# Kernel tuning notes

Hardware: AMD Instinct MI355X
Metric: run time of the kernel (lower is better)

The kernel has to match this reference:

```python
import jax, jax.numpy as jnp
import numpy as np

EMBED_DIM = 1024
ATTN_DIM = 128
B, S = 4, 2048


def setup_inputs() -> dict:
    key = jax.random.key(0)
    k1, k2, k3, k4 = jax.random.split(key, 4)
    embedded = jax.random.normal(k1, (B, S, EMBED_DIM), dtype=jnp.float32)
    # torch nn.Linear weights are [out_features, in_features]
    scale = 1.0 / np.sqrt(EMBED_DIM)
    Wk = jax.random.uniform(k2, (ATTN_DIM, EMBED_DIM), dtype=jnp.float32, minval=-scale, maxval=scale)
    Wq = jax.random.uniform(k3, (ATTN_DIM, EMBED_DIM), dtype=jnp.float32, minval=-scale, maxval=scale)
    Wv = jax.random.uniform(k4, (ATTN_DIM, EMBED_DIM), dtype=jnp.float32, minval=-scale, maxval=scale)
    return {"embedded": embedded, "Wk": Wk, "Wq": Wq, "Wv": Wv}


def reference(embedded, Wk, Wq, Wv):
    # projections (no bias): x @ W.T
    k = jnp.einsum('bse,ae->bsa', embedded, Wk)  # [B,S,A]
    q = jnp.einsum('bse,ae->bsa', embedded, Wq)
    v = jnp.einsum('bse,ae->bsa', embedded, Wv)
    ad = k.shape[-1]
    scores = jnp.einsum('bqa,bka->bqk', q, k) / jnp.sqrt(jnp.float32(ad))  # [B,S,S]
    causal = jnp.tril(jnp.ones((scores.shape[1], scores.shape[1]), dtype=bool))
    scores = jnp.where(causal, scores, -jnp.inf)
    probs = jax.nn.softmax(scores, axis=-1)
    out = jnp.einsum('bqk,bka->bqa', probs, v)
    return jnp.round(out, 4)
```

## Files before the change

### kernel.cpp

```cpp
#include <hip/hip_runtime.h>
#include <hip/hip_bf16.h>
#include <math.h>

#define B 4
#define S 2048
#define E 1024
#define A 128
#define CHUNK 256
#define NCHMAX 8

typedef __attribute__((ext_vector_type(8))) short short8;
typedef __attribute__((ext_vector_type(4))) float floatx4;

static __device__ __forceinline__ short f2bf(float f) {
  union { float f; unsigned u; } c;
  c.f = f;
  unsigned r = (c.u + 0x7fffu + ((c.u >> 16) & 1u)) >> 16;
  return (short)r;
}
static __device__ __forceinline__ unsigned f2bf2(float x, float y) {
  __hip_bfloat162 h = __float22bfloat162_rn(float2{x, y});
  union { __hip_bfloat162 h; unsigned u; } c;
  c.h = h;
  return c.u;
}

#define PJ 72
__global__ __launch_bounds__(256) void proj_gemm(
    const float* __restrict__ X,
    const float* __restrict__ Wq,
    const float* __restrict__ Wk,
    const float* __restrict__ Wv,
    short* __restrict__ Qbf,
    short* __restrict__ Kbf,
    short* __restrict__ Vt) {
  __shared__ short As[64 * PJ];
  __shared__ short Bs[128 * PJ];

  const int m0 = blockIdx.x * 64;
  const int which = blockIdx.y;
  const float* Wp = (which == 0) ? Wq : (which == 1) ? Wk : Wv;

  const int tid = threadIdx.x;
  const int wave = tid >> 6;
  const int lane = tid & 63;
  const int mh = wave & 1;
  const int nh = wave >> 1;
  const int l16 = lane & 15;
  const int quad = lane >> 4;

  floatx4 acc[2][4] = {};

  for (int k0 = 0; k0 < E; k0 += 64) {
#pragma unroll
    for (int i = 0; i < 4; ++i) {
      const int f = tid + i * 256;
      const int row = f >> 4, c4 = f & 15;
      const float4 v = *(const float4*)&X[(size_t)(m0 + row) * E + k0 + c4 * 4];
      uint2 p; p.x = f2bf2(v.x, v.y); p.y = f2bf2(v.z, v.w);
      *(uint2*)&As[row * PJ + c4 * 4] = p;
    }
#pragma unroll
    for (int i = 0; i < 8; ++i) {
      const int f = tid + i * 256;
      const int row = f >> 4, c4 = f & 15;
      const float4 v = *(const float4*)&Wp[(size_t)row * E + k0 + c4 * 4];
      uint2 p; p.x = f2bf2(v.x, v.y); p.y = f2bf2(v.z, v.w);
      *(uint2*)&Bs[row * PJ + c4 * 4] = p;
    }
    __syncthreads();

    short8 afr[2][2], bfr[4][2];
#pragma unroll
    for (int ms = 0; ms < 2; ++ms)
#pragma unroll
      for (int ks = 0; ks < 2; ++ks)
        afr[ms][ks] = *(const short8*)&As[(mh * 32 + ms * 16 + l16) * PJ + ks * 32 + quad * 8];
#pragma unroll
    for (int nt = 0; nt < 4; ++nt)
#pragma unroll
      for (int ks = 0; ks < 2; ++ks)
        bfr[nt][ks] = *(const short8*)&Bs[(nh * 64 + nt * 16 + l16) * PJ + ks * 32 + quad * 8];

#pragma unroll
    for (int ms = 0; ms < 2; ++ms)
#pragma unroll
      for (int nt = 0; nt < 4; ++nt)
#pragma unroll
        for (int ks = 0; ks < 2; ++ks)
          acc[ms][nt] = __builtin_amdgcn_mfma_f32_16x16x32_bf16(
              afr[ms][ks], bfr[nt][ks], acc[ms][nt], 0, 0, 0);
    __syncthreads();
  }

  const float qscale = 0.08838834764831845f;
#pragma unroll
  for (int ms = 0; ms < 2; ++ms) {
#pragma unroll
    for (int nt = 0; nt < 4; ++nt) {
      const int n = nh * 64 + nt * 16 + l16;
      const int mbase = m0 + mh * 32 + ms * 16 + quad * 4;
      if (which == 2) {
        const int b = mbase >> 11, s = mbase & (S - 1);
        short4 p;
        p.x = f2bf(acc[ms][nt][0]); p.y = f2bf(acc[ms][nt][1]);
        p.z = f2bf(acc[ms][nt][2]); p.w = f2bf(acc[ms][nt][3]);
        *(short4*)&Vt[((size_t)b * A + n) * S + s] = p;
      } else {
        short* Outp = (which == 0) ? Qbf : Kbf;
        const float sc = (which == 0) ? qscale : 1.0f;
#pragma unroll
        for (int r = 0; r < 4; ++r)
          Outp[(size_t)(mbase + r) * A + n] = f2bf(acc[ms][nt][r] * sc);
      }
    }
  }
}

#define LK 132
#define LV 68
__global__ __launch_bounds__(256) void attn_part(
    const short* __restrict__ Qbf,
    const short* __restrict__ Kbf,
    const short* __restrict__ Vt,
    float* __restrict__ Opart,
    float* __restrict__ Lpart) {
  __shared__ short Ks[64 * LK];
  __shared__ short Vs[128 * LV];
  __shared__ short Ps[4][16 * LV];

  const int rev = (int)gridDim.x - 1 - (int)blockIdx.x;
  const int qt = rev >> 3;
  const int chunk = rev & 7;
  const int b = qt >> 5;
  const int q0 = (qt & 31) << 6;
  const int nk = q0 + 64;
  const int kstart = chunk * CHUNK;
  if (kstart >= nk) return;
  const int kend = min(kstart + CHUNK, nk);

  const int tid = threadIdx.x;
  const int wave = tid >> 6;
  const int lane = tid & 63;
  const int l16 = lane & 15;
  const int quad = lane >> 4;

  short8 qfr[4];
  {
    const size_t qrow = (size_t)(b * S + q0 + wave * 16 + l16);
#pragma unroll
    for (int ks = 0; ks < 4; ++ks)
      qfr[ks] = *(const short8*)&Qbf[qrow * A + ks * 32 + quad * 8];
  }

  float l_acc[4] = {0.f, 0.f, 0.f, 0.f};
  floatx4 oacc[8] = {};

  const int myrow = q0 + wave * 16 + quad * 4;
  const short* Kbase = Kbf + (size_t)b * S * A;
  const short* Vbase = Vt + (size_t)b * A * S;

  for (int j0 = kstart; j0 < kend; j0 += 64) {
#pragma unroll
    for (int i = 0; i < 4; ++i) {
      const int f = tid + i * 256;
      const int row = f >> 4, c8 = f & 15;
      *(short8*)&Ks[row * LK + c8 * 8] =
          *(const short8*)&Kbase[(size_t)(j0 + row) * A + c8 * 8];
    }
#pragma unroll
    for (int i = 0; i < 4; ++i) {
      const int f = tid + i * 256;
      const int ar = f >> 3, c8 = f & 7;
      *(short8*)&Vs[ar * LV + c8 * 8] =
          *(const short8*)&Vbase[(size_t)ar * S + j0 + c8 * 8];
    }
    __syncthreads();

    floatx4 sc[4];
#pragma unroll
    for (int nt = 0; nt < 4; ++nt) {
      floatx4 c = {};
#pragma unroll
      for (int ks = 0; ks < 4; ++ks) {
        const short8 bfr = *(const short8*)&Ks[(nt * 16 + l16) * LK + ks * 32 + quad * 8];
        c = __builtin_amdgcn_mfma_f32_16x16x32_bf16(qfr[ks], bfr, c, 0, 0, 0);
      }
      sc[nt] = c;
    }

#pragma unroll
    for (int nt = 0; nt < 4; ++nt) {
      const int key = j0 + nt * 16 + l16;
#pragma unroll
      for (int r = 0; r < 4; ++r) {
        const float p = (key > myrow + r) ? 0.f : __expf(sc[nt][r]);
        sc[nt][r] = p;
        l_acc[r] += p;
      }
    }

#pragma unroll
    for (int nt = 0; nt < 4; ++nt)
#pragma unroll
      for (int r = 0; r < 4; ++r)
        Ps[wave][(quad * 4 + r) * LV + nt * 16 + l16] = f2bf(sc[nt][r]);

    short8 pfr[2];
#pragma unroll
    for (int ks = 0; ks < 2; ++ks)
      pfr[ks] = *(const short8*)&Ps[wave][l16 * LV + ks * 32 + quad * 8];

#pragma unroll
    for (int nt = 0; nt < 8; ++nt) {
#pragma unroll
      for (int ks = 0; ks < 2; ++ks) {
        const short8 vfr = *(const short8*)&Vs[(nt * 16 + l16) * LV + ks * 32 + quad * 8];
        oacc[nt] = __builtin_amdgcn_mfma_f32_16x16x32_bf16(pfr[ks], vfr, oacc[nt], 0, 0, 0);
      }
    }
    __syncthreads();
  }

  const int slot = qt * NCHMAX + chunk;
  float* op = Opart + (size_t)slot * 64 * 128;
  const int lr = wave * 16 + quad * 4;
#pragma unroll
  for (int nt = 0; nt < 8; ++nt)
#pragma unroll
    for (int r = 0; r < 4; ++r)
      op[(lr + r) * 128 + nt * 16 + l16] = oacc[nt][r];

#pragma unroll
  for (int r = 0; r < 4; ++r) {
    float l = l_acc[r];
    l += __shfl_xor(l, 1);
    l += __shfl_xor(l, 2);
    l += __shfl_xor(l, 4);
    l += __shfl_xor(l, 8);
    if (l16 == 0) Lpart[slot * 64 + lr + r] = l;
  }
}

__global__ __launch_bounds__(256) void attn_reduce(
    const float* __restrict__ Opart,
    const float* __restrict__ Lpart,
    float* __restrict__ Out) {
  const int qt = blockIdx.x;
  const int b = qt >> 5;
  const int q0 = (qt & 31) << 6;
  const int nch = (q0 + 64 + CHUNK - 1) / CHUNK;

  const int tid = threadIdx.x;
  const int lr = tid >> 2;
  const int c0 = (tid & 3) * 32;

  float ltot = 0.f;
  for (int c = 0; c < nch; ++c) ltot += Lpart[(qt * NCHMAX + c) * 64 + lr];
  const float inv = 1.f / ltot;

  float4 acc[8] = {};
  for (int c = 0; c < nch; ++c) {
    const float4* op = (const float4*)
        (Opart + ((size_t)(qt * NCHMAX + c) * 64 + lr) * 128 + c0);
#pragma unroll
    for (int i = 0; i < 8; ++i) {
      const float4 v = op[i];
      acc[i].x += v.x; acc[i].y += v.y; acc[i].z += v.z; acc[i].w += v.w;
    }
  }

  float4* o = (float4*)(Out + (size_t)(b * S + q0 + lr) * A + c0);
#pragma unroll
  for (int i = 0; i < 8; ++i) {
    float4 v = acc[i];
    v.x *= inv; v.y *= inv; v.z *= inv; v.w *= inv;
    o[i] = v;
  }
}

extern "C" void kernel_launch(void* const* d_in, const int* in_sizes, int n_in,
                              void* d_out, int out_size, void* d_ws, size_t ws_size,
                              hipStream_t stream) {
  const float* X  = (const float*)d_in[0];
  const float* Wk = (const float*)d_in[1];
  const float* Wq = (const float*)d_in[2];
  const float* Wv = (const float*)d_in[3];
  float* Out = (float*)d_out;

  const size_t qkv_elems = (size_t)B * S * A;
  short* Qbf = (short*)d_ws;
  short* Kbf = Qbf + qkv_elems;
  short* Vt  = Kbf + qkv_elems;
  float* Opart = (float*)(Vt + qkv_elems);
  float* Lpart = Opart + (size_t)1024 * 64 * 128;

  dim3 pgrid(B * S / 64, 3);
  proj_gemm<<<pgrid, 256, 0, stream>>>(X, Wq, Wk, Wv, Qbf, Kbf, Vt);
  attn_part<<<(B * S / 64) * NCHMAX, 256, 0, stream>>>(Qbf, Kbf, Vt, Opart, Lpart);
  attn_reduce<<<B * S / 64, 256, 0, stream>>>(Opart, Lpart, Out);
}
```

Measured before the change: 136.4 us.

## Compute transposed scores to keep P in registers; pre-convert weights to bf16

The attention kernel now computes S^T (K as the A operand, Q as B), so each lane holds four consecutive keys for one query. It packs exp values straight into bf16 fragments and feeds them to 16x16x16 MFMAs against V, which removes the per-wave LDS round trip for P and the extra barrier-free shuffle of probabilities. A separate small kernel converts the weights to bf16 once per call, so the projection GEMM loads half the bytes and skips per-block conversion. The costs are an extra kernel launch and smaller-K MFMAs (16x16x16) with more instructions for the PV product.

After: 143.8 us. +5.5%, slower.

```diff
diff --git a/kernel.cpp b/kernel.cpp
--- a/kernel.cpp
+++ b/kernel.cpp
@@ -9,8 +9,24 @@
 #define CHUNK 256
 #define NCHMAX 8
 
+typedef __attribute__((ext_vector_type(4))) short shortx4;
 typedef __attribute__((ext_vector_type(8))) short short8;
 typedef __attribute__((ext_vector_type(4))) float floatx4;
+
+#if defined(__has_builtin)
+#if __has_builtin(__builtin_amdgcn_mfma_f32_16x16x16bf16_1k)
+#define MFMA16(Av, Bv, Cv) __builtin_amdgcn_mfma_f32_16x16x16bf16_1k((Av), (Bv), (Cv), 0, 0, 0)
+#endif
+#endif
+#ifndef MFMA16
+static __device__ __forceinline__ floatx4 mfma16_asm(shortx4 a, shortx4 b, floatx4 c) {
+  floatx4 d;
+  asm volatile("v_mfma_f32_16x16x16_bf16 %0, %1, %2, %3"
+               : "=v"(d) : "v"(a), "v"(b), "v"(c));
+  return d;
+}
+#define MFMA16(Av, Bv, Cv) mfma16_asm((Av), (Bv), (Cv))
+#endif
 
 static __device__ __forceinline__ short f2bf(float f) {
   union { float f; unsigned u; } c;
@@ -25,12 +41,24 @@
   return c.u;
 }
 
+__global__ __launch_bounds__(256) void wconv(
+    const float* __restrict__ Wq,
+    const float* __restrict__ Wk,
+    const float* __restrict__ Wv,
+    short* __restrict__ Wbf) {
+  const int which = blockIdx.y;
+  const float* Wp = (which == 0) ? Wq : (which == 1) ? Wk : Wv;
+  short* o = Wbf + (size_t)which * A * E;
+  const int f = blockIdx.x * 256 + threadIdx.x;
+  const float4 v = *(const float4*)&Wp[(size_t)f * 4];
+  uint2 p; p.x = f2bf2(v.x, v.y); p.y = f2bf2(v.z, v.w);
+  *(uint2*)&o[(size_t)f * 4] = p;
+}
+
 #define PJ 72
 __global__ __launch_bounds__(256) void proj_gemm(
     const float* __restrict__ X,
-    const float* __restrict__ Wq,
-    const float* __restrict__ Wk,
-    const float* __restrict__ Wv,
+    const short* __restrict__ Wbf,
     short* __restrict__ Qbf,
     short* __restrict__ Kbf,
     short* __restrict__ Vt) {
@@ -39,7 +67,7 @@
 
   const int m0 = blockIdx.x * 64;
   const int which = blockIdx.y;
-  const float* Wp = (which == 0) ? Wq : (which == 1) ? Wk : Wv;
+  const short* Wpb = Wbf + (size_t)which * A * E;
 
   const int tid = threadIdx.x;
   const int wave = tid >> 6;
@@ -61,12 +89,11 @@
       *(uint2*)&As[row * PJ + c4 * 4] = p;
     }
 #pragma unroll
-    for (int i = 0; i < 8; ++i) {
+    for (int i = 0; i < 4; ++i) {
       const int f = tid + i * 256;
-      const int row = f >> 4, c4 = f & 15;
-      const float4 v = *(const float4*)&Wp[(size_t)row * E + k0 + c4 * 4];
-      uint2 p; p.x = f2bf2(v.x, v.y); p.y = f2bf2(v.z, v.w);
-      *(uint2*)&Bs[row * PJ + c4 * 4] = p;
+      const int row = f >> 3, c8 = f & 7;
+      *(short8*)&Bs[row * PJ + c8 * 8] =
+          *(const short8*)&Wpb[(size_t)row * E + k0 + c8 * 8];
     }
     __syncthreads();
 
@@ -127,7 +154,6 @@
     float* __restrict__ Lpart) {
   __shared__ short Ks[64 * LK];
   __shared__ short Vs[128 * LV];
-  __shared__ short Ps[4][16 * LV];
 
   const int rev = (int)gridDim.x - 1 - (int)blockIdx.x;
   const int qt = rev >> 3;
@@ -145,18 +171,19 @@
   const int l16 = lane & 15;
   const int quad = lane >> 4;
 
+  const int qrow = q0 + wave * 16 + l16;
+
   short8 qfr[4];
   {
-    const size_t qrow = (size_t)(b * S + q0 + wave * 16 + l16);
+    const size_t qr = (size_t)(b * S + qrow);
 #pragma unroll
     for (int ks = 0; ks < 4; ++ks)
-      qfr[ks] = *(const short8*)&Qbf[qrow * A + ks * 32 + quad * 8];
-  }
-
-  float l_acc[4] = {0.f, 0.f, 0.f, 0.f};
-  floatx4 oacc[8] = {};
-
-  const int myrow = q0 + wave * 16 + quad * 4;
+      qfr[ks] = *(const short8*)&Qbf[qr * A + ks * 32 + quad * 8];
+  }
+
+  float l_acc = 0.f;
+  floatx4 oaccT[8] = {};
+
   const short* Kbase = Kbf + (size_t)b * S * A;
   const short* Vbase = Vt + (size_t)b * A * S;
 
@@ -177,69 +204,50 @@
     }
     __syncthreads();
 
-    floatx4 sc[4];
 #pragma unroll
     for (int nt = 0; nt < 4; ++nt) {
-      floatx4 c = {};
+      floatx4 st = {};
 #pragma unroll
       for (int ks = 0; ks < 4; ++ks) {
-        const short8 bfr = *(const short8*)&Ks[(nt * 16 + l16) * LK + ks * 32 + quad * 8];
-        c = __builtin_amdgcn_mfma_f32_16x16x32_bf16(qfr[ks], bfr, c, 0, 0, 0);
+        const short8 kfr = *(const short8*)&Ks[(nt * 16 + l16) * LK + ks * 32 + quad * 8];
+        st = __builtin_amdgcn_mfma_f32_16x16x32_bf16(kfr, qfr[ks], st, 0, 0, 0);
       }
-      sc[nt] = c;
-    }
-
-#pragma unroll
-    for (int nt = 0; nt < 4; ++nt) {
-      const int key = j0 + nt * 16 + l16;
+      float pr[4];
 #pragma unroll
       for (int r = 0; r < 4; ++r) {
-        const float p = (key > myrow + r) ? 0.f : __expf(sc[nt][r]);
-        sc[nt][r] = p;
-        l_acc[r] += p;
+        const int key = j0 + nt * 16 + quad * 4 + r;
+        const float p = (key > qrow) ? 0.f : __expf(st[r]);
+        pr[r] = p;
+        l_acc += p;
       }
-    }
-
-#pragma unroll
-    for (int nt = 0; nt < 4; ++nt)
-#pragma unroll
-      for (int r = 0; r < 4; ++r)
-        Ps[wave][(quad * 4 + r) * LV + nt * 16 + l16] = f2bf(sc[nt][r]);
-
-    short8 pfr[2];
-#pragma unroll
-    for (int ks = 0; ks < 2; ++ks)
-      pfr[ks] = *(const short8*)&Ps[wave][l16 * LV + ks * 32 + quad * 8];
-
-#pragma unroll
-    for (int nt = 0; nt < 8; ++nt) {
-#pragma unroll
-      for (int ks = 0; ks < 2; ++ks) {
-        const short8 vfr = *(const short8*)&Vs[(nt * 16 + l16) * LV + ks * 32 + quad * 8];
-        oacc[nt] = __builtin_amdgcn_mfma_f32_16x16x32_bf16(pfr[ks], vfr, oacc[nt], 0, 0, 0);
+      union { uint2 u; shortx4 s; } pk;
+      pk.u.x = f2bf2(pr[0], pr[1]);
+      pk.u.y = f2bf2(pr[2], pr[3]);
+      const shortx4 pfrB = pk.s;
+
+#pragma unroll
+      for (int at = 0; at < 8; ++at) {
+        const shortx4 vfr = *(const shortx4*)&Vs[(at * 16 + l16) * LV + nt * 16 + quad * 4];
+        oaccT[at] = MFMA16(vfr, pfrB, oaccT[at]);
       }
     }
     __syncthreads();
   }
+
+  l_acc += __shfl_xor(l_acc, 16);
+  l_acc += __shfl_xor(l_acc, 32);
 
   const int slot = qt * NCHMAX + chunk;
   float* op = Opart + (size_t)slot * 64 * 128;
-  const int lr = wave * 16 + quad * 4;
-#pragma unroll
-  for (int nt = 0; nt < 8; ++nt)
-#pragma unroll
-    for (int r = 0; r < 4; ++r)
-      op[(lr + r) * 128 + nt * 16 + l16] = oacc[nt][r];
-
-#pragma unroll
-  for (int r = 0; r < 4; ++r) {
-    float l = l_acc[r];
-    l += __shfl_xor(l, 1);
-    l += __shfl_xor(l, 2);
-    l += __shfl_xor(l, 4);
-    l += __shfl_xor(l, 8);
-    if (l16 == 0) Lpart[slot * 64 + lr + r] = l;
-  }
+  const int lr = wave * 16 + l16;
+#pragma unroll
+  for (int at = 0; at < 8; ++at) {
+    float4 v;
+    v.x = oaccT[at][0]; v.y = oaccT[at][1];
+    v.z = oaccT[at][2]; v.w = oaccT[at][3];
+    *(float4*)&op[(size_t)lr * 128 + at * 16 + quad * 4] = v;
+  }
+  if (quad == 0) Lpart[slot * 64 + lr] = l_acc;
 }
 
 __global__ __launch_bounds__(256) void attn_reduce(
@@ -294,9 +302,11 @@
   short* Vt  = Kbf + qkv_elems;
   float* Opart = (float*)(Vt + qkv_elems);
   float* Lpart = Opart + (size_t)1024 * 64 * 128;
-
+  short* Wbf = (short*)(Lpart + (size_t)1024 * 64);
+
+  wconv<<<dim3(A * E / 4 / 256, 3), 256, 0, stream>>>(Wq, Wk, Wv, Wbf);
   dim3 pgrid(B * S / 64, 3);
-  proj_gemm<<<pgrid, 256, 0, stream>>>(X, Wq, Wk, Wv, Qbf, Kbf, Vt);
+  proj_gemm<<<pgrid, 256, 0, stream>>>(X, Wbf, Qbf, Kbf, Vt);
   attn_part<<<(B * S / 64) * NCHMAX, 256, 0, stream>>>(Qbf, Kbf, Vt, Opart, Lpart);
   attn_reduce<<<B * S / 64, 256, 0, stream>>>(Opart, Lpart, Out);
 }
```

## Pre-convert weights to bf16 and register-prefetch next tiles in GEMM and attention

Applied to the files above, without the earlier changes.

Adds a small kernel that converts the three projection weight matrices to bf16 once per call, so the projection GEMM loads half as many weight bytes and skips per-tile conversion. Both the projection GEMM and the attention partial kernel now prefetch the next K-step tile into registers while MFMAs run on the current shared-memory tile, with the barrier moved to the top of the loop. This trades extra register pressure and one more kernel launch for more overlap of global loads with compute.

After: 131.5 us. 1.04x faster.

```diff
diff --git a/kernel.cpp b/kernel.cpp
--- a/kernel.cpp
+++ b/kernel.cpp
@@ -25,12 +25,24 @@
   return c.u;
 }
 
+__global__ __launch_bounds__(256) void wconv(
+    const float* __restrict__ Wq,
+    const float* __restrict__ Wk,
+    const float* __restrict__ Wv,
+    short* __restrict__ Wbf) {
+  const int which = blockIdx.y;
+  const float* Wp = (which == 0) ? Wq : (which == 1) ? Wk : Wv;
+  short* o = Wbf + (size_t)which * A * E;
+  const int f = blockIdx.x * 256 + threadIdx.x;
+  const float4 v = *(const float4*)&Wp[(size_t)f * 4];
+  uint2 p; p.x = f2bf2(v.x, v.y); p.y = f2bf2(v.z, v.w);
+  *(uint2*)&o[(size_t)f * 4] = p;
+}
+
 #define PJ 72
 __global__ __launch_bounds__(256) void proj_gemm(
     const float* __restrict__ X,
-    const float* __restrict__ Wq,
-    const float* __restrict__ Wk,
-    const float* __restrict__ Wv,
+    const short* __restrict__ Wbf,
     short* __restrict__ Qbf,
     short* __restrict__ Kbf,
     short* __restrict__ Vt) {
@@ -39,7 +51,7 @@
 
   const int m0 = blockIdx.x * 64;
   const int which = blockIdx.y;
-  const float* Wp = (which == 0) ? Wq : (which == 1) ? Wk : Wv;
+  const short* Wpb = Wbf + (size_t)which * A * E;
 
   const int tid = threadIdx.x;
   const int wave = tid >> 6;
@@ -49,26 +61,42 @@
   const int l16 = lane & 15;
   const int quad = lane >> 4;
 
+  int arow[4], ac4[4], brow[4], bc8[4];
+#pragma unroll
+  for (int i = 0; i < 4; ++i) {
+    const int fa = tid + i * 256;
+    arow[i] = fa >> 4; ac4[i] = fa & 15;
+    const int fb = tid + i * 256;
+    brow[i] = fb >> 3; bc8[i] = fb & 7;
+  }
+
   floatx4 acc[2][4] = {};
+  float4 aplf[4];
+  short8 bplf[4];
+
+#pragma unroll
+  for (int i = 0; i < 4; ++i) {
+    aplf[i] = *(const float4*)&X[(size_t)(m0 + arow[i]) * E + ac4[i] * 4];
+    bplf[i] = *(const short8*)&Wpb[(size_t)brow[i] * E + bc8[i] * 8];
+  }
 
   for (int k0 = 0; k0 < E; k0 += 64) {
+    __syncthreads();
 #pragma unroll
     for (int i = 0; i < 4; ++i) {
-      const int f = tid + i * 256;
-      const int row = f >> 4, c4 = f & 15;
-      const float4 v = *(const float4*)&X[(size_t)(m0 + row) * E + k0 + c4 * 4];
-      uint2 p; p.x = f2bf2(v.x, v.y); p.y = f2bf2(v.z, v.w);
-      *(uint2*)&As[row * PJ + c4 * 4] = p;
-    }
-#pragma unroll
-    for (int i = 0; i < 8; ++i) {
-      const int f = tid + i * 256;
-      const int row = f >> 4, c4 = f & 15;
-      const float4 v = *(const float4*)&Wp[(size_t)row * E + k0 + c4 * 4];
-      uint2 p; p.x = f2bf2(v.x, v.y); p.y = f2bf2(v.z, v.w);
-      *(uint2*)&Bs[row * PJ + c4 * 4] = p;
+      uint2 p; p.x = f2bf2(aplf[i].x, aplf[i].y); p.y = f2bf2(aplf[i].z, aplf[i].w);
+      *(uint2*)&As[arow[i] * PJ + ac4[i] * 4] = p;
+      *(short8*)&Bs[brow[i] * PJ + bc8[i] * 8] = bplf[i];
     }
     __syncthreads();
+
+    if (k0 + 64 < E) {
+#pragma unroll
+      for (int i = 0; i < 4; ++i) {
+        aplf[i] = *(const float4*)&X[(size_t)(m0 + arow[i]) * E + (k0 + 64) + ac4[i] * 4];
+        bplf[i] = *(const short8*)&Wpb[(size_t)brow[i] * E + (k0 + 64) + bc8[i] * 8];
+      }
+    }
 
     short8 afr[2][2], bfr[4][2];
 #pragma unroll
@@ -90,7 +118,6 @@
         for (int ks = 0; ks < 2; ++ks)
           acc[ms][nt] = __builtin_amdgcn_mfma_f32_16x16x32_bf16(
               afr[ms][ks], bfr[nt][ks], acc[ms][nt], 0, 0, 0);
-    __syncthreads();
   }
 
   const float qscale = 0.08838834764831845f;
@@ -145,6 +172,14 @@
   const int l16 = lane & 15;
   const int quad = lane >> 4;
 
+  int krow[4], kc8[4], vrow[4], vc8[4];
+#pragma unroll
+  for (int i = 0; i < 4; ++i) {
+    const int f = tid + i * 256;
+    krow[i] = f >> 4; kc8[i] = f & 15;
+    vrow[i] = f >> 3; vc8[i] = f & 7;
+  }
+
   short8 qfr[4];
   {
     const size_t qrow = (size_t)(b * S + q0 + wave * 16 + l16);
@@ -160,22 +195,29 @@
   const short* Kbase = Kbf + (size_t)b * S * A;
   const short* Vbase = Vt + (size_t)b * A * S;
 
+  short8 kplf[4], vplf[4];
+#pragma unroll
+  for (int i = 0; i < 4; ++i) {
+    kplf[i] = *(const short8*)&Kbase[(size_t)(kstart + krow[i]) * A + kc8[i] * 8];
+    vplf[i] = *(const short8*)&Vbase[(size_t)vrow[i] * S + kstart + vc8[i] * 8];
+  }
+
   for (int j0 = kstart; j0 < kend; j0 += 64) {
+    __syncthreads();
 #pragma unroll
     for (int i = 0; i < 4; ++i) {
-      const int f = tid + i * 256;
-      const int row = f >> 4, c8 = f & 15;
-      *(short8*)&Ks[row * LK + c8 * 8] =
-          *(const short8*)&Kbase[(size_t)(j0 + row) * A + c8 * 8];
-    }
-#pragma unroll
-    for (int i = 0; i < 4; ++i) {
-      const int f = tid + i * 256;
-      const int ar = f >> 3, c8 = f & 7;
-      *(short8*)&Vs[ar * LV + c8 * 8] =
-          *(const short8*)&Vbase[(size_t)ar * S + j0 + c8 * 8];
+      *(short8*)&Ks[krow[i] * LK + kc8[i] * 8] = kplf[i];
+      *(short8*)&Vs[vrow[i] * LV + vc8[i] * 8] = vplf[i];
     }
     __syncthreads();
+
+    if (j0 + 64 < kend) {
+#pragma unroll
+      for (int i = 0; i < 4; ++i) {
+        kplf[i] = *(const short8*)&Kbase[(size_t)(j0 + 64 + krow[i]) * A + kc8[i] * 8];
+        vplf[i] = *(const short8*)&Vbase[(size_t)vrow[i] * S + j0 + 64 + vc8[i] * 8];
+      }
+    }
 
     floatx4 sc[4];
 #pragma unroll
@@ -219,7 +261,6 @@
         oacc[nt] = __builtin_amdgcn_mfma_f32_16x16x32_bf16(pfr[ks], vfr, oacc[nt], 0, 0, 0);
       }
     }
-    __syncthreads();
   }
 
   const int slot = qt * NCHMAX + chunk;
@@ -294,9 +335,11 @@
   short* Vt  = Kbf + qkv_elems;
   float* Opart = (float*)(Vt + qkv_elems);
   float* Lpart = Opart + (size_t)1024 * 64 * 128;
-
+  short* Wbf = (short*)(Lpart + (size_t)1024 * 64);
+
+  wconv<<<dim3(A * E / 4 / 256, 3), 256, 0, stream>>>(Wq, Wk, Wv, Wbf);
   dim3 pgrid(B * S / 64, 3);
-  proj_gemm<<<pgrid, 256, 0, stream>>>(X, Wq, Wk, Wv, Qbf, Kbf, Vt);
+  proj_gemm<<<pgrid, 256, 0, stream>>>(X, Wbf, Qbf, Kbf, Vt);
   attn_part<<<(B * S / 64) * NCHMAX, 256, 0, stream>>>(Qbf, Kbf, Vt, Opart, Lpart);
   attn_reduce<<<B * S / 64, 256, 0, stream>>>(Opart, Lpart, Out);
 }
```
